# Kernel tuning notes

Hardware: AMD Instinct MI355X
Metric: run time of the kernel (lower is better)

The kernel has to match this reference:

```python
import jax, jax.numpy as jnp
import numpy as np

LN_EPS = 1e-5
RMS_EPS = 1.1920929e-07  # torch.finfo(float32).eps (RMSNorm default eps=None)


def _layernorm(x, g, b):
    m = jnp.mean(x, axis=-1, keepdims=True)
    xc = x - m
    v = jnp.mean(xc * xc, axis=-1, keepdims=True)
    return xc / jnp.sqrt(v + LN_EPS) * g + b


def setup_inputs() -> dict:
    key = jax.random.key(0)
    ks = jax.random.split(key, 8)
    L, D, H, M, B, S = 4, 512, 8, 2048, 4, 2048
    std = 0.02
    return {
        "x": jax.random.normal(ks[0], (B, S, D), dtype=jnp.float32),
        # torch nn.Linear weights are [out, in]
        "Wq": jax.random.normal(ks[1], (L, D, D), dtype=jnp.float32) * std,
        "Wk": jax.random.normal(ks[2], (L, D, D), dtype=jnp.float32) * std,
        "Wv": jax.random.normal(ks[3], (L, D, D), dtype=jnp.float32) * std,
        "rms_w": jnp.ones((L, H, D // H), dtype=jnp.float32),
        "Wo": jax.random.normal(ks[4], (L, D, D), dtype=jnp.float32) * std,
        "bo": jnp.zeros((L, D), dtype=jnp.float32),
        "diffw": jnp.full((L,), 0.2, dtype=jnp.float32),
        "g_ffn": jnp.ones((L, D), dtype=jnp.float32),
        "b_ffn": jnp.zeros((L, D), dtype=jnp.float32),
        "W1": jax.random.normal(ks[5], (L, M, D), dtype=jnp.float32) * std,
        "b1": jnp.zeros((L, M), dtype=jnp.float32),
        "W2": jax.random.normal(ks[6], (L, D, M), dtype=jnp.float32) * std,
        "b2": jnp.zeros((L, D), dtype=jnp.float32),
        "g_f": jnp.ones((D,), dtype=jnp.float32),
        "b_f": jnp.zeros((D,), dtype=jnp.float32),
    }


def reference(x, Wq, Wk, Wv, rms_w, Wo, bo, diffw, g_ffn, b_ffn, W1, b1, W2, b2, g_f, b_f):
    def layer(xc, p):
        wq, wk, wv, rw, wo, bob, dw, g1, bn1, w1, bb1, w2, bb2 = p
        B, S, D = xc.shape
        H = rw.shape[0]
        F = D // (2 * H)  # per-component head dim (q/k split in two)
        qs = (xc @ wq.T).reshape(B, S, H, 2, F)
        ks_ = (xc @ wk.T).reshape(B, S, H, 2, F)
        scores = jnp.einsum('bqhif,bkhif->ibhqk', qs, ks_) * (F ** -0.5)
        atts = jax.nn.softmax(scores, axis=-1)  # [2,B,H,S,S]
        att = atts[0] - dw * atts[1]  # differential attention
        vs = (xc @ wv.T).reshape(B, S, H, D // H)
        o = jnp.einsum('bhqk,bkhe->bqhe', att, vs)  # [B,S,H,D/H]
        # fused per-token RMSNorm over (heads, head_dim)
        o = o / jnp.sqrt(jnp.mean(o * o, axis=(-2, -1), keepdims=True) + RMS_EPS) * rw
        xa = (o.reshape(B, S, D) @ wo.T + bob) * (1.0 - dw)
        xc = xa + xc  # attn residual
        h = _layernorm(xc, g1, bn1)
        h = jax.nn.gelu(h @ w1.T + bb1, approximate=False)
        xc = (h @ w2.T + bb2) + xc  # ffn residual
        return xc, None

    xf, _ = jax.lax.scan(layer, x, (Wq, Wk, Wv, rms_w, Wo, bo, diffw, g_ffn, b_ffn, W1, b1, W2, b2))
    return _layernorm(xf, g_f, b_f)
```

## Files before the change

### kernel.cpp

```cpp
#include <hip/hip_runtime.h>
#include <math.h>

#define B_ 4
#define S_ 2048
#define D_ 512
#define H_ 8
#define E_ 64
#define M_ 2048
#define L_ 4
#define R_ (B_ * S_)
#define RD_ ((size_t)R_ * D_)

typedef unsigned short u16;
typedef short short8 __attribute__((ext_vector_type(8)));
typedef float f32x4 __attribute__((ext_vector_type(4)));

__device__ __forceinline__ float4 ldg4(const float* p) {
    return *reinterpret_cast<const float4*>(p);
}
__device__ __forceinline__ float gelu_f(float x) {
    return 0.5f * x * (1.0f + erff(x * 0.70710678118654752440f));
}
__device__ __forceinline__ unsigned int cvt_pk_bf16(float lo, float hi) {
    unsigned int r;
    asm("v_cvt_pk_bf16_f32 %0, %1, %2" : "=v"(r) : "v"(lo), "v"(hi));
    return r;
}
__device__ __forceinline__ float fast_exp2(float x) {
    return __builtin_amdgcn_exp2f(x);
}
__device__ __forceinline__ float bf2f(u16 u) {
    union { unsigned int i; float f; } v; v.i = ((unsigned int)u) << 16;
    return v.f;
}
__device__ __forceinline__ void async_copy16(const u16* g, u16* l) {
    auto* gp = reinterpret_cast<const __attribute__((address_space(1))) unsigned int*>(
        reinterpret_cast<uintptr_t>(g));
    auto* lp = reinterpret_cast<__attribute__((address_space(3))) unsigned int*>(
        reinterpret_cast<uintptr_t>(l));
    __builtin_amdgcn_global_load_lds(gp, lp, 16, 0, 0);
}

template <int EPI, int NB>
__global__ __launch_bounds__(256) void gemm_bf16(
    const u16* __restrict__ A, const u16* __restrict__ W,
    const float* __restrict__ bias, const float* __restrict__ res,
    const float* __restrict__ dwp, float* __restrict__ Cf,
    u16* __restrict__ Cb, int M, int N, int K, int ldc)
{
    constexpr int TN = NB / 32;
    __shared__ __align__(16) u16 As[2][128 * 32];
    __shared__ __align__(16) u16 Bs[2][NB * 32];

    const int t  = threadIdx.x;
    const int w  = t >> 6, l = t & 63;
    const int lr = l & 15, g = l >> 4;
    const int wr = (w >> 1) * 64, wc = (w & 1) * (NB / 2);
    const int bm = blockIdx.x * 128, bn = blockIdx.y * NB;

    const u16* gA0 = A + (size_t)(bm + (t >> 2)) * K + (t & 3) * 8;
    const u16* gA1 = A + (size_t)(bm + 64 + (t >> 2)) * K + (t & 3) * 8;
    const u16* gB0 = W + (size_t)(bn + (t >> 2)) * K + (t & 3) * 8;
    const u16* gB1 = gB0;
    if constexpr (NB == 128) gB1 = W + (size_t)(bn + 64 + (t >> 2)) * K + (t & 3) * 8;

    f32x4 acc[4][TN];
#pragma unroll
    for (int m = 0; m < 4; ++m)
#pragma unroll
        for (int n = 0; n < TN; ++n) acc[m][n] = (f32x4){0.f, 0.f, 0.f, 0.f};

    {
        u16* ab = &As[0][0];
        async_copy16(gA0, ab + w * 512);
        async_copy16(gA1, ab + 2048 + w * 512);
        u16* bb = &Bs[0][0];
        async_copy16(gB0, bb + w * 512);
        if constexpr (NB == 128) async_copy16(gB1, bb + 2048 + w * 512);
    }
    __syncthreads();

    const int NT = K >> 5;
    int cur = 0;
    for (int kt = 0; kt < NT; ++kt) {
        if (kt + 1 < NT) {
            const int off = (kt + 1) << 5;
            u16* ab = &As[cur ^ 1][0];
            async_copy16(gA0 + off, ab + w * 512);
            async_copy16(gA1 + off, ab + 2048 + w * 512);
            u16* bb = &Bs[cur ^ 1][0];
            async_copy16(gB0 + off, bb + w * 512);
            if constexpr (NB == 128) async_copy16(gB1 + off, bb + 2048 + w * 512);
        }
        short8 af[4], bfv[TN];
#pragma unroll
        for (int m = 0; m < 4; ++m)
            af[m] = *reinterpret_cast<const short8*>(&As[cur][(wr + m * 16 + lr) * 32 + g * 8]);
#pragma unroll
        for (int n = 0; n < TN; ++n)
            bfv[n] = *reinterpret_cast<const short8*>(&Bs[cur][(wc + n * 16 + lr) * 32 + g * 8]);
#pragma unroll
        for (int m = 0; m < 4; ++m)
#pragma unroll
            for (int n = 0; n < TN; ++n)
                acc[m][n] = __builtin_amdgcn_mfma_f32_16x16x32_bf16(af[m], bfv[n], acc[m][n], 0, 0, 0);
        __syncthreads();
        cur ^= 1;
    }

    float sc1 = 1.f;
    if constexpr (EPI == 1) sc1 = 1.f - dwp[0];
    float bcolv[TN];
#pragma unroll
    for (int n = 0; n < TN; ++n) bcolv[n] = 0.f;
    if constexpr (EPI >= 1) {
#pragma unroll
        for (int n = 0; n < TN; ++n) bcolv[n] = bias[bn + wc + n * 16 + lr];
    }
#pragma unroll
    for (int m = 0; m < 4; ++m) {
        const int row0 = bm + wr + m * 16 + g * 4;
#pragma unroll
        for (int n = 0; n < TN; ++n) {
            const int col = bn + wc + n * 16 + lr;
            float vv[4];
#pragma unroll
            for (int q = 0; q < 4; ++q) {
                const int row = row0 + q;
                float v = acc[m][n][q];
                if constexpr (EPI >= 1) v += bcolv[n];
                if constexpr (EPI == 1) v = v * sc1 + res[(size_t)row * N + col];
                if constexpr (EPI == 2) v = gelu_f(v);
                if constexpr (EPI == 3) v += res[(size_t)row * N + col];
                if constexpr (EPI == 1 || EPI == 3) Cf[(size_t)row * N + col] = v;
                vv[q] = v;
            }
            const unsigned int pa = cvt_pk_bf16(vv[0], vv[1]);
            const unsigned int pb = cvt_pk_bf16(vv[2], vv[3]);
            Cb[(size_t)(row0 + 0) * ldc + col] = (u16)pa;
            Cb[(size_t)(row0 + 1) * ldc + col] = (u16)(pa >> 16);
            Cb[(size_t)(row0 + 2) * ldc + col] = (u16)pb;
            Cb[(size_t)(row0 + 3) * ldc + col] = (u16)(pb >> 16);
        }
    }
}

#define LDSW 72
#define QKVLD 1536
__global__ __launch_bounds__(512) void attn_mfma(
    const u16* __restrict__ QKV, u16* __restrict__ O,
    const float* __restrict__ dwp)
{
    __shared__ __align__(16) u16 Ks[64][LDSW];
    __shared__ __align__(16) u16 Vt[64][LDSW];
    __shared__ __align__(16) u16 Ps[128][LDSW];

    const int t   = threadIdx.x;
    const int w   = t >> 6;
    const int l   = t & 63;
    const int lr  = l & 15;
    const int g   = l >> 4;
    const int lk8 = g << 3;

    const int d   = blockIdx.y * 16 + blockIdx.x;
    const int s   = d >> 3;
    const int bh  = (d & 7) * 4 + (s >> 4);
    const int qt  = s & 15;
    const int b   = bh >> 3, h = bh & 7;

    const float dw = dwp[0];
    const float C = 0.17677669529663687f * 1.44269504088896340736f;
    const size_t tokbase = (size_t)b * S_;

    const u16* qrow = QKV + (tokbase + (size_t)(qt * 128 + w * 16 + lr)) * QKVLD + h * E_;
    short8 qf[2];
    {
        short8 qr0 = *reinterpret_cast<const short8*>(qrow + lk8);
        short8 qr1 = *reinterpret_cast<const short8*>(qrow + 32 + lk8);
        uint4 u0, u1;
        u0.x = cvt_pk_bf16(bf2f((u16)qr0[0]) * C, bf2f((u16)qr0[1]) * C);
        u0.y = cvt_pk_bf16(bf2f((u16)qr0[2]) * C, bf2f((u16)qr0[3]) * C);
        u0.z = cvt_pk_bf16(bf2f((u16)qr0[4]) * C, bf2f((u16)qr0[5]) * C);
        u0.w = cvt_pk_bf16(bf2f((u16)qr0[6]) * C, bf2f((u16)qr0[7]) * C);
        u1.x = cvt_pk_bf16(bf2f((u16)qr1[0]) * C, bf2f((u16)qr1[1]) * C);
        u1.y = cvt_pk_bf16(bf2f((u16)qr1[2]) * C, bf2f((u16)qr1[3]) * C);
        u1.z = cvt_pk_bf16(bf2f((u16)qr1[4]) * C, bf2f((u16)qr1[5]) * C);
        u1.w = cvt_pk_bf16(bf2f((u16)qr1[6]) * C, bf2f((u16)qr1[7]) * C);
        qf[0] = *reinterpret_cast<short8*>(&u0);
        qf[1] = *reinterpret_cast<short8*>(&u1);
    }

    float lsum[2] = {0.f, 0.f};
    f32x4 oacc[2][4];
#pragma unroll
    for (int c = 0; c < 2; ++c)
#pragma unroll
        for (int et = 0; et < 4; ++et) oacc[c][et] = (f32x4){0.f, 0.f, 0.f, 0.f};

    const int sr   = t >> 3;
    const int sc0  = (t & 7) << 3;
    const int prow = w * 16 + lr;
    const int vbit = lr & 8;

    const u16* kbase = QKV + tokbase * QKVLD + h * E_ + 512 + sc0;

    {
        const u16* kp = kbase + (size_t)sr * QKVLD;
        short8 kv = *reinterpret_cast<const short8*>(kp);
        short8 vv = *reinterpret_cast<const short8*>(kp + 512);
        *reinterpret_cast<short8*>(&Ks[sr][sc0]) = kv;
        const int vcol = sr ^ sc0;
#pragma unroll
        for (int i = 0; i < 8; ++i)
            Vt[sc0 + i][vcol] = (u16)vv[i];
    }
    __syncthreads();

    const int NT = S_ / 64;
    short8 kv_n, vv_n;
    for (int kt = 0; kt < NT; ++kt) {
        const bool pf = (kt + 1 < NT);
        if (pf) {
            const u16* kp = kbase + (size_t)((kt + 1) * 64 + sr) * QKVLD;
            kv_n = *reinterpret_cast<const short8*>(kp);
            vv_n = *reinterpret_cast<const short8*>(kp + 512);
        }

        short8 vfr[4][2];
#pragma unroll
        for (int et = 0; et < 4; ++et) {
            const int vx = (et << 4) ^ vbit;
            vfr[et][0] = *reinterpret_cast<const short8*>(&Vt[et * 16 + lr][lk8 ^ vx]);
            vfr[et][1] = *reinterpret_cast<const short8*>(&Vt[et * 16 + lr][(32 + lk8) ^ vx]);
        }

#pragma unroll
        for (int c = 0; c < 2; ++c) {
            f32x4 sacc[4];
            const f32x4 zf = (f32x4){0.f, 0.f, 0.f, 0.f};
#pragma unroll
            for (int kc = 0; kc < 4; ++kc) {
                short8 kf = *reinterpret_cast<const short8*>(&Ks[kc * 16 + lr][c * 32 + lk8]);
                sacc[kc] = __builtin_amdgcn_mfma_f32_16x16x32_bf16(kf, qf[c], zf, 0, 0, 0);
            }
            float ls = 0.f;
#pragma unroll
            for (int kc = 0; kc < 4; ++kc) {
                float p0 = fast_exp2(sacc[kc][0]);
                float p1 = fast_exp2(sacc[kc][1]);
                float p2 = fast_exp2(sacc[kc][2]);
                float p3 = fast_exp2(sacc[kc][3]);
                ls += (p0 + p1) + (p2 + p3);
                uint2 pk;
                pk.x = cvt_pk_bf16(p0, p1);
                pk.y = cvt_pk_bf16(p2, p3);
                *reinterpret_cast<uint2*>(&Ps[prow][kc * 16 + (g << 2)]) = pk;
            }
            lsum[c] += ls;
            short8 pf0 = *reinterpret_cast<const short8*>(&Ps[prow][lk8]);
            short8 pf1 = *reinterpret_cast<const short8*>(&Ps[prow][32 + lk8]);
#pragma unroll
            for (int et = 0; et < 4; ++et) {
                oacc[c][et] = __builtin_amdgcn_mfma_f32_16x16x32_bf16(vfr[et][0], pf0, oacc[c][et], 0, 0, 0);
                oacc[c][et] = __builtin_amdgcn_mfma_f32_16x16x32_bf16(vfr[et][1], pf1, oacc[c][et], 0, 0, 0);
            }
        }

        if (pf) {
            __syncthreads();
            *reinterpret_cast<short8*>(&Ks[sr][sc0]) = kv_n;
            const int vcol = sr ^ sc0;
#pragma unroll
            for (int i = 0; i < 8; ++i)
                Vt[sc0 + i][vcol] = (u16)vv_n[i];
            __syncthreads();
        }
    }

#pragma unroll
    for (int c = 0; c < 2; ++c) {
        lsum[c] += __shfl_xor(lsum[c], 16, 64);
        lsum[c] += __shfl_xor(lsum[c], 32, 64);
    }
    const float inv0 = 1.f / lsum[0];
    const float inv1 = dw / lsum[1];

    const size_t row = tokbase + (size_t)(qt * 128 + w * 16 + lr);
    u16* op = O + row * D_ + h * E_ + (g << 2);
#pragma unroll
    for (int et = 0; et < 4; ++et) {
        uint2 ov;
        ov.x = cvt_pk_bf16(oacc[0][et][0] * inv0 - oacc[1][et][0] * inv1,
                           oacc[0][et][1] * inv0 - oacc[1][et][1] * inv1);
        ov.y = cvt_pk_bf16(oacc[0][et][2] * inv0 - oacc[1][et][2] * inv1,
                           oacc[0][et][3] * inv0 - oacc[1][et][3] * inv1);
        *reinterpret_cast<uint2*>(op + et * 16) = ov;
    }
}

__global__ __launch_bounds__(256) void rmsnorm_bf(
    u16* __restrict__ X, const float* __restrict__ rw)
{
    const int row  = (blockIdx.x << 2) + (threadIdx.x >> 6);
    const int lane = threadIdx.x & 63;
    u16* xp = X + (size_t)row * D_ + lane * 8;
    short8 xv = *reinterpret_cast<const short8*>(xp);
    float xf[8];
#pragma unroll
    for (int i = 0; i < 8; ++i) xf[i] = bf2f((u16)xv[i]);
    float q = 0.f;
#pragma unroll
    for (int i = 0; i < 8; ++i) q += xf[i] * xf[i];
#pragma unroll
    for (int o = 1; o < 64; o <<= 1) q += __shfl_xor(q, o, 64);
    const float rstd = rsqrtf(q * (1.0f / 512.0f) + 1.1920929e-07f);
    const float* wp = rw + lane * 8;
    float4 w0 = ldg4(wp), w1 = ldg4(wp + 4);
    uint4 yv;
    yv.x = cvt_pk_bf16(xf[0] * rstd * w0.x, xf[1] * rstd * w0.y);
    yv.y = cvt_pk_bf16(xf[2] * rstd * w0.z, xf[3] * rstd * w0.w);
    yv.z = cvt_pk_bf16(xf[4] * rstd * w1.x, xf[5] * rstd * w1.y);
    yv.w = cvt_pk_bf16(xf[6] * rstd * w1.z, xf[7] * rstd * w1.w);
    *reinterpret_cast<uint4*>(xp) = yv;
}

template <int OUT>
__global__ __launch_bounds__(256) void layernorm_k(
    const float* __restrict__ X, const float* __restrict__ g,
    const float* __restrict__ bb, float* __restrict__ Yf,
    u16* __restrict__ Yb, float eps)
{
    const int row  = (blockIdx.x << 2) + (threadIdx.x >> 6);
    const int lane = threadIdx.x & 63;
    const float* xp = X + (size_t)row * D_;
    float4 x0 = ldg4(xp + lane * 4);
    float4 x1 = ldg4(xp + 256 + lane * 4);

    float s = x0.x + x0.y + x0.z + x0.w + x1.x + x1.y + x1.z + x1.w;
#pragma unroll
    for (int o = 1; o < 64; o <<= 1) s += __shfl_xor(s, o, 64);
    const float mean = s * (1.0f / 512.0f);

    x0.x -= mean; x0.y -= mean; x0.z -= mean; x0.w -= mean;
    x1.x -= mean; x1.y -= mean; x1.z -= mean; x1.w -= mean;
    float q = x0.x * x0.x + x0.y * x0.y + x0.z * x0.z + x0.w * x0.w
            + x1.x * x1.x + x1.y * x1.y + x1.z * x1.z + x1.w * x1.w;
#pragma unroll
    for (int o = 1; o < 64; o <<= 1) q += __shfl_xor(q, o, 64);
    const float rstd = rsqrtf(q * (1.0f / 512.0f) + eps);

    float4 g0 = ldg4(g + lane * 4),  g1 = ldg4(g + 256 + lane * 4);
    float4 b0 = ldg4(bb + lane * 4), b1 = ldg4(bb + 256 + lane * 4);
    float y[8];
    y[0] = x0.x * rstd * g0.x + b0.x; y[1] = x0.y * rstd * g0.y + b0.y;
    y[2] = x0.z * rstd * g0.z + b0.z; y[3] = x0.w * rstd * g0.w + b0.w;
    y[4] = x1.x * rstd * g1.x + b1.x; y[5] = x1.y * rstd * g1.y + b1.y;
    y[6] = x1.z * rstd * g1.z + b1.z; y[7] = x1.w * rstd * g1.w + b1.w;
    if constexpr (OUT == 0) {
        float* yp = Yf + (size_t)row * D_;
        *reinterpret_cast<float4*>(yp + lane * 4)       = make_float4(y[0], y[1], y[2], y[3]);
        *reinterpret_cast<float4*>(yp + 256 + lane * 4) = make_float4(y[4], y[5], y[6], y[7]);
    } else {
        u16* yp = Yb + (size_t)row * D_;
        uint2 a, b;
        a.x = cvt_pk_bf16(y[0], y[1]); a.y = cvt_pk_bf16(y[2], y[3]);
        b.x = cvt_pk_bf16(y[4], y[5]); b.y = cvt_pk_bf16(y[6], y[7]);
        *reinterpret_cast<uint2*>(yp + lane * 4)       = a;
        *reinterpret_cast<uint2*>(yp + 256 + lane * 4) = b;
    }
}

__global__ __launch_bounds__(256) void initcvt(
    const float* __restrict__ x, float* __restrict__ xc, u16* __restrict__ xcb)
{
    const size_t i = ((size_t)blockIdx.x * 256 + threadIdx.x) * 4;
    float4 v = ldg4(x + i);
    *reinterpret_cast<float4*>(xc + i) = v;
    uint2 o;
    o.x = cvt_pk_bf16(v.x, v.y); o.y = cvt_pk_bf16(v.z, v.w);
    *reinterpret_cast<uint2*>(xcb + i) = o;
}

__global__ __launch_bounds__(256) void conv_layer_w(
    const float* __restrict__ Wq, const float* __restrict__ Wk,
    const float* __restrict__ Wv, const float* __restrict__ Wo,
    const float* __restrict__ W1, const float* __restrict__ W2,
    u16* __restrict__ wqkv, u16* __restrict__ wo,
    u16* __restrict__ w1, u16* __restrict__ w2)
{
    const size_t i = ((size_t)blockIdx.x * 256 + threadIdx.x) * 4;
    const float* src; u16* dst;
    if (i < 786432) {
        dst = wqkv + i;
        if (i < 262144)      src = Wq + i;
        else if (i < 524288) src = Wk + (i - 262144);
        else                 src = Wv + (i - 524288);
    } else if (i < 1048576) { src = Wo + (i - 786432);  dst = wo + (i - 786432); }
    else if (i < 2097152)   { src = W1 + (i - 1048576); dst = w1 + (i - 1048576); }
    else                    { src = W2 + (i - 2097152); dst = w2 + (i - 2097152); }
    float4 v = ldg4(src);
    uint2 o;
    o.x = cvt_pk_bf16(v.x, v.y); o.y = cvt_pk_bf16(v.z, v.w);
    *reinterpret_cast<uint2*>(dst) = o;
}

extern "C" void kernel_launch(void* const* d_in, const int* in_sizes, int n_in,
                              void* d_out, int out_size, void* d_ws, size_t ws_size,
                              hipStream_t stream)
{
    const float* x     = (const float*)d_in[0];
    const float* Wq    = (const float*)d_in[1];
    const float* Wk    = (const float*)d_in[2];
    const float* Wv    = (const float*)d_in[3];
    const float* rms_w = (const float*)d_in[4];
    const float* Wo    = (const float*)d_in[5];
    const float* bo    = (const float*)d_in[6];
    const float* diffw = (const float*)d_in[7];
    const float* g_ffn = (const float*)d_in[8];
    const float* b_ffn = (const float*)d_in[9];
    const float* W1    = (const float*)d_in[10];
    const float* b1    = (const float*)d_in[11];
    const float* W2    = (const float*)d_in[12];
    const float* b2    = (const float*)d_in[13];
    const float* g_f   = (const float*)d_in[14];
    const float* b_f   = (const float*)d_in[15];

    char* ws = (char*)d_ws;
    float* xc   = (float*)(ws);
    u16*   xcb  = (u16*)(ws + 16777216);
    u16*   qkvb = (u16*)(ws + 25165824);
    u16*   ob   = (u16*)(ws + 50331648);
    u16*   tb   = qkvb;
    u16*   hb   = (u16*)(ws + 33554432);
    u16*   wqkv = (u16*)(ws + 67108864);
    u16*   wo_b = (u16*)(ws + 68681728);
    u16*   w1_b = (u16*)(ws + 69206016);
    u16*   w2_b = (u16*)(ws + 71303168);

    const dim3 blk(256);
    initcvt<<<dim3(RD_ / 4 / 256), blk, 0, stream>>>(x, xc, xcb);

    const dim3 g_tok(R_ / 4);

    for (int l = 0; l < L_; ++l) {
        const float* bo_l = bo + (size_t)l * D_;
        const float* b1_l = b1 + (size_t)l * M_;
        const float* b2_l = b2 + (size_t)l * D_;
        const float* dw_l = diffw + l;

        conv_layer_w<<<dim3(3072), blk, 0, stream>>>(
            Wq + (size_t)l * D_ * D_, Wk + (size_t)l * D_ * D_,
            Wv + (size_t)l * D_ * D_, Wo + (size_t)l * D_ * D_,
            W1 + (size_t)l * M_ * D_, W2 + (size_t)l * D_ * M_,
            wqkv, wo_b, w1_b, w2_b);

        gemm_bf16<0, 128><<<dim3(R_ / 128, 12), blk, 0, stream>>>(
            xcb, wqkv, nullptr, nullptr, nullptr, nullptr, qkvb,
            R_, 1536, D_, 1536);

        attn_mfma<<<dim3(S_ / 128, B_ * H_), dim3(512), 0, stream>>>(qkvb, ob, dw_l);

        rmsnorm_bf<<<g_tok, blk, 0, stream>>>(ob, rms_w + (size_t)l * D_);

        gemm_bf16<1, 64><<<dim3(R_ / 128, 8), blk, 0, stream>>>(
            ob, wo_b, bo_l, xc, dw_l, xc, xcb, R_, D_, D_, D_);

        layernorm_k<1><<<g_tok, blk, 0, stream>>>(
            xc, g_ffn + (size_t)l * D_, b_ffn + (size_t)l * D_, nullptr, tb, 1e-5f);

        gemm_bf16<2, 128><<<dim3(R_ / 128, 16), blk, 0, stream>>>(
            tb, w1_b, b1_l, nullptr, nullptr, nullptr, hb, R_, M_, D_, M_);

        gemm_bf16<3, 64><<<dim3(R_ / 128, 8), blk, 0, stream>>>(
            hb, w2_b, b2_l, xc, nullptr, xc, xcb, R_, D_, M_, D_);
    }

    layernorm_k<0><<<g_tok, blk, 0, stream>>>(xc, g_f, b_f, (float*)d_out, nullptr, 1e-5f);
}
```

Before: 788.1 us.

## Parameterize GEMM K-tile and double-buffer attention K/V shared memory

```diff
diff --git a/kernel.cpp b/kernel.cpp
--- a/kernel.cpp
+++ b/kernel.cpp
@@ -41,16 +41,22 @@
     __builtin_amdgcn_global_load_lds(gp, lp, 16, 0, 0);
 }
 
-template <int EPI, int NB>
+template <int EPI, int NB, int BK>
 __global__ __launch_bounds__(256) void gemm_bf16(
     const u16* __restrict__ A, const u16* __restrict__ W,
     const float* __restrict__ bias, const float* __restrict__ res,
     const float* __restrict__ dwp, float* __restrict__ Cf,
     u16* __restrict__ Cb, int M, int N, int K, int ldc)
 {
-    constexpr int TN = NB / 32;
-    __shared__ __align__(16) u16 As[2][128 * 32];
-    __shared__ __align__(16) u16 Bs[2][NB * 32];
+    constexpr int TN  = NB / 32;
+    constexpr int KK  = BK / 32;
+    constexpr int C8  = BK / 8;
+    constexpr int NA  = (128 * BK) / 2048;
+    constexpr int NBc = (NB * BK) / 2048;
+    constexpr int RSTEP = 2048 / BK;
+
+    __shared__ __align__(16) u16 As[2][128 * BK];
+    __shared__ __align__(16) u16 Bs[2][NB * BK];
 
     const int t  = threadIdx.x;
     const int w  = t >> 6, l = t & 63;
@@ -58,52 +64,65 @@
     const int wr = (w >> 1) * 64, wc = (w & 1) * (NB / 2);
     const int bm = blockIdx.x * 128, bn = blockIdx.y * NB;
 
-    const u16* gA0 = A + (size_t)(bm + (t >> 2)) * K + (t & 3) * 8;
-    const u16* gA1 = A + (size_t)(bm + 64 + (t >> 2)) * K + (t & 3) * 8;
-    const u16* gB0 = W + (size_t)(bn + (t >> 2)) * K + (t & 3) * 8;
-    const u16* gB1 = gB0;
-    if constexpr (NB == 128) gB1 = W + (size_t)(bn + 64 + (t >> 2)) * K + (t & 3) * 8;
+    const int crow = t / C8;
+    const int ccol = (t % C8) * 8;
 
     f32x4 acc[4][TN];
 #pragma unroll
     for (int m = 0; m < 4; ++m)
 #pragma unroll
         for (int n = 0; n < TN; ++n) acc[m][n] = (f32x4){0.f, 0.f, 0.f, 0.f};
+
+    const u16* gA = A + (size_t)(bm + crow) * K + ccol;
+    const u16* gB = W + (size_t)(bn + crow) * K + ccol;
 
     {
         u16* ab = &As[0][0];
-        async_copy16(gA0, ab + w * 512);
-        async_copy16(gA1, ab + 2048 + w * 512);
+#pragma unroll
+        for (int k = 0; k < NA; ++k)
+            async_copy16(gA + (size_t)(k * RSTEP) * K, ab + (t + 256 * k) * 8);
         u16* bb = &Bs[0][0];
-        async_copy16(gB0, bb + w * 512);
-        if constexpr (NB == 128) async_copy16(gB1, bb + 2048 + w * 512);
+#pragma unroll
+        for (int k = 0; k < NBc; ++k)
+            async_copy16(gB + (size_t)(k * RSTEP) * K, bb + (t + 256 * k) * 8);
     }
     __syncthreads();
 
-    const int NT = K >> 5;
+    const int NT = K / BK;
     int cur = 0;
     for (int kt = 0; kt < NT; ++kt) {
         if (kt + 1 < NT) {
-            const int off = (kt + 1) << 5;
+            const int off = (kt + 1) * BK;
             u16* ab = &As[cur ^ 1][0];
-            async_copy16(gA0 + off, ab + w * 512);
-            async_copy16(gA1 + off, ab + 2048 + w * 512);
+#pragma unroll
+            for (int k = 0; k < NA; ++k)
+                async_copy16(gA + (size_t)(k * RSTEP) * K + off, ab + (t + 256 * k) * 8);
             u16* bb = &Bs[cur ^ 1][0];
-            async_copy16(gB0 + off, bb + w * 512);
-            if constexpr (NB == 128) async_copy16(gB1 + off, bb + 2048 + w * 512);
-        }
-        short8 af[4], bfv[TN];
+#pragma unroll
+            for (int k = 0; k < NBc; ++k)
+                async_copy16(gB + (size_t)(k * RSTEP) * K + off, bb + (t + 256 * k) * 8);
+        }
+        short8 af[4][KK], bfv[TN][KK];
 #pragma unroll
         for (int m = 0; m < 4; ++m)
-            af[m] = *reinterpret_cast<const short8*>(&As[cur][(wr + m * 16 + lr) * 32 + g * 8]);
+#pragma unroll
+            for (int kk = 0; kk < KK; ++kk)
+                af[m][kk] = *reinterpret_cast<const short8*>(
+                    &As[cur][(wr + m * 16 + lr) * BK + kk * 32 + g * 8]);
 #pragma unroll
         for (int n = 0; n < TN; ++n)
-            bfv[n] = *reinterpret_cast<const short8*>(&Bs[cur][(wc + n * 16 + lr) * 32 + g * 8]);
-#pragma unroll
-        for (int m = 0; m < 4; ++m)
-#pragma unroll
-            for (int n = 0; n < TN; ++n)
-                acc[m][n] = __builtin_amdgcn_mfma_f32_16x16x32_bf16(af[m], bfv[n], acc[m][n], 0, 0, 0);
+#pragma unroll
+            for (int kk = 0; kk < KK; ++kk)
+                bfv[n][kk] = *reinterpret_cast<const short8*>(
+                    &Bs[cur][(wc + n * 16 + lr) * BK + kk * 32 + g * 8]);
+#pragma unroll
+        for (int kk = 0; kk < KK; ++kk)
+#pragma unroll
+            for (int m = 0; m < 4; ++m)
+#pragma unroll
+                for (int n = 0; n < TN; ++n)
+                    acc[m][n] = __builtin_amdgcn_mfma_f32_16x16x32_bf16(
+                        af[m][kk], bfv[n][kk], acc[m][n], 0, 0, 0);
         __syncthreads();
         cur ^= 1;
     }
@@ -151,8 +170,8 @@
     const u16* __restrict__ QKV, u16* __restrict__ O,
     const float* __restrict__ dwp)
 {
-    __shared__ __align__(16) u16 Ks[64][LDSW];
-    __shared__ __align__(16) u16 Vt[64][LDSW];
+    __shared__ __align__(16) u16 Ks[2][64][LDSW];
+    __shared__ __align__(16) u16 Vt[2][64][LDSW];
     __shared__ __align__(16) u16 Ps[128][LDSW];
 
     const int t   = threadIdx.x;
@@ -201,6 +220,7 @@
     const int sc0  = (t & 7) << 3;
     const int prow = w * 16 + lr;
     const int vbit = lr & 8;
+    const int vcol = sr ^ sc0;
 
     const u16* kbase = QKV + tokbase * QKVLD + h * E_ + 512 + sc0;
 
@@ -208,15 +228,15 @@
         const u16* kp = kbase + (size_t)sr * QKVLD;
         short8 kv = *reinterpret_cast<const short8*>(kp);
         short8 vv = *reinterpret_cast<const short8*>(kp + 512);
-        *reinterpret_cast<short8*>(&Ks[sr][sc0]) = kv;
-        const int vcol = sr ^ sc0;
+        *reinterpret_cast<short8*>(&Ks[0][sr][sc0]) = kv;
 #pragma unroll
         for (int i = 0; i < 8; ++i)
-            Vt[sc0 + i][vcol] = (u16)vv[i];
+            Vt[0][sc0 + i][vcol] = (u16)vv[i];
     }
     __syncthreads();
 
     const int NT = S_ / 64;
+    int cur = 0;
     short8 kv_n, vv_n;
     for (int kt = 0; kt < NT; ++kt) {
         const bool pf = (kt + 1 < NT);
@@ -230,8 +250,8 @@
 #pragma unroll
         for (int et = 0; et < 4; ++et) {
             const int vx = (et << 4) ^ vbit;
-            vfr[et][0] = *reinterpret_cast<const short8*>(&Vt[et * 16 + lr][lk8 ^ vx]);
-            vfr[et][1] = *reinterpret_cast<const short8*>(&Vt[et * 16 + lr][(32 + lk8) ^ vx]);
+            vfr[et][0] = *reinterpret_cast<const short8*>(&Vt[cur][et * 16 + lr][lk8 ^ vx]);
+            vfr[et][1] = *reinterpret_cast<const short8*>(&Vt[cur][et * 16 + lr][(32 + lk8) ^ vx]);
         }
 
 #pragma unroll
@@ -240,7 +260,7 @@
             const f32x4 zf = (f32x4){0.f, 0.f, 0.f, 0.f};
 #pragma unroll
             for (int kc = 0; kc < 4; ++kc) {
-                short8 kf = *reinterpret_cast<const short8*>(&Ks[kc * 16 + lr][c * 32 + lk8]);
+                short8 kf = *reinterpret_cast<const short8*>(&Ks[cur][kc * 16 + lr][c * 32 + lk8]);
                 sacc[kc] = __builtin_amdgcn_mfma_f32_16x16x32_bf16(kf, qf[c], zf, 0, 0, 0);
             }
             float ls = 0.f;
@@ -267,14 +287,13 @@
         }
 
         if (pf) {
+            *reinterpret_cast<short8*>(&Ks[cur ^ 1][sr][sc0]) = kv_n;
+#pragma unroll
+            for (int i = 0; i < 8; ++i)
+                Vt[cur ^ 1][sc0 + i][vcol] = (u16)vv_n[i];
             __syncthreads();
-            *reinterpret_cast<short8*>(&Ks[sr][sc0]) = kv_n;
-            const int vcol = sr ^ sc0;
-#pragma unroll
-            for (int i = 0; i < 8; ++i)
-                Vt[sc0 + i][vcol] = (u16)vv_n[i];
-            __syncthreads();
-        }
+        }
+        cur ^= 1;
     }
 
 #pragma unroll
@@ -454,7 +473,7 @@
             W1 + (size_t)l * M_ * D_, W2 + (size_t)l * D_ * M_,
             wqkv, wo_b, w1_b, w2_b);
 
-        gemm_bf16<0, 128><<<dim3(R_ / 128, 12), blk, 0, stream>>>(
+        gemm_bf16<0, 128, 32><<<dim3(R_ / 128, 12), blk, 0, stream>>>(
             xcb, wqkv, nullptr, nullptr, nullptr, nullptr, qkvb,
             R_, 1536, D_, 1536);
 
@@ -462,16 +481,16 @@
 
         rmsnorm_bf<<<g_tok, blk, 0, stream>>>(ob, rms_w + (size_t)l * D_);
 
-        gemm_bf16<1, 64><<<dim3(R_ / 128, 8), blk, 0, stream>>>(
+        gemm_bf16<1, 64, 64><<<dim3(R_ / 128, 8), blk, 0, stream>>>(
             ob, wo_b, bo_l, xc, dw_l, xc, xcb, R_, D_, D_, D_);
 
         layernorm_k<1><<<g_tok, blk, 0, stream>>>(
             xc, g_ffn + (size_t)l * D_, b_ffn + (size_t)l * D_, nullptr, tb, 1e-5f);
 
-        gemm_bf16<2, 128><<<dim3(R_ / 128, 16), blk, 0, stream>>>(
+        gemm_bf16<2, 128, 32><<<dim3(R_ / 128, 16), blk, 0, stream>>>(
             tb, w1_b, b1_l, nullptr, nullptr, nullptr, hb, R_, M_, D_, M_);
 
-        gemm_bf16<3, 64><<<dim3(R_ / 128, 8), blk, 0, stream>>>(
+        gemm_bf16<3, 64, 64><<<dim3(R_ / 128, 8), blk, 0, stream>>>(
             hb, w2_b, b2_l, xc, nullptr, xc, xcb, R_, D_, M_, D_);
     }
 
```

Measured after the change: 778.1 us. No clear change (-1.3%).
